# Kernel optimization log

Measured on AMD Instinct MI355X. Metric: run time of the kernel, lower is better.

The kernel has to match this reference:

```python
import jax, jax.numpy as jnp
import numpy as np


def setup_inputs() -> dict:
    key = jax.random.key(0)
    b, d, s = 16, 1024, 4096
    x = jax.random.normal(key, (b, d, s), dtype=jnp.float32)
    return {"x": x, "k": 8}


def reference(x, k):
    # k-max pooling over the last axis, preserving original relative order.
    # torch: topk -> argsort(ind) -> gather. Equivalent: take top-k values,
    # then reorder them by ascending original index.
    vals, idx = jax.lax.top_k(x, k)            # [b, d, k]
    order = jnp.argsort(idx, axis=-1)          # positions that sort original indices ascending
    out = jnp.take_along_axis(vals, order, axis=-1)  # [b, d, k] in original order
    return out
```

## Files before the change

### kernel.cpp

```cpp
#include <hip/hip_runtime.h>
#include <stdint.h>

#define WPB    4
#define CAP    96
#define KK     8
#define SLEN   4096
#define CHUNKS 16

__global__ __launch_bounds__(256, 4)
void kmax_kernel(const float* __restrict__ x, float* __restrict__ out, int nrows) {
    const int wave = threadIdx.x >> 6;
    const int lane = threadIdx.x & 63;
    const int row  = blockIdx.x * WPB + wave;
    const bool active = row < nrows;

    __shared__ int   s_cnt[WPB];
    __shared__ float s_val[WPB][CAP];
    __shared__ int   s_idx[WPB][CAP];

    if (lane == 0) s_cnt[wave] = 0;
    __syncthreads();

    const float NEG_INF = __int_as_float(0xff800000);

    float Tthr = 0.0f;
    float4 f[CHUNKS];

    if (active) {
        const float4* xr = reinterpret_cast<const float4*>(x + (size_t)row * SLEN);
        #pragma unroll
        for (int j = 0; j < CHUNKS; ++j)
            f[j] = xr[j * 64 + lane];

        float m[8];
        #pragma unroll
        for (int e = 0; e < 8; ++e) m[e] = NEG_INF;
        #pragma unroll
        for (int j = 0; j < CHUNKS; ++j) {
            const int b = (j & 1) * 4;
            m[b + 0] = fmaxf(m[b + 0], f[j].x);
            m[b + 1] = fmaxf(m[b + 1], f[j].y);
            m[b + 2] = fmaxf(m[b + 2], f[j].z);
            m[b + 3] = fmaxf(m[b + 3], f[j].w);
        }

        #define MCAS(a, b) { float hi = fmaxf(m[a], m[b]); float lo = fminf(m[a], m[b]); m[a] = hi; m[b] = lo; }
        MCAS(0,1) MCAS(2,3) MCAS(4,5) MCAS(6,7)
        MCAS(0,2) MCAS(1,3) MCAS(4,6) MCAS(5,7)
        MCAS(1,2) MCAS(5,6)
        MCAS(0,4) MCAS(1,5) MCAS(2,6) MCAS(3,7)
        MCAS(2,4) MCAS(3,5)
        MCAS(1,2) MCAS(3,4) MCAS(5,6)
        #undef MCAS

        #pragma unroll
        for (int t = 0; t < KK; ++t) {
            float r = m[0];
            #pragma unroll
            for (int off = 32; off >= 1; off >>= 1)
                r = fmaxf(r, __shfl_xor(r, off, 64));
            const bool win = (m[0] == r);
            m[0] = win ? m[1] : m[0];
            m[1] = win ? m[2] : m[1];
            m[2] = win ? m[3] : m[2];
            m[3] = win ? m[4] : m[3];
            m[4] = win ? m[5] : m[4];
            m[5] = win ? m[6] : m[5];
            m[6] = win ? m[7] : m[6];
            m[7] = win ? NEG_INF : m[7];
            Tthr = r;
        }

        #pragma unroll
        for (int j = 0; j < CHUNKS; ++j) {
            const float4 v = f[j];
            const bool p0 = v.x >= Tthr, p1 = v.y >= Tthr, p2 = v.z >= Tthr, p3 = v.w >= Tthr;
            if (p0 || p1 || p2 || p3) {
                const int base = (j * 64 + lane) * 4;
                if (p0) { int p = atomicAdd(&s_cnt[wave], 1); if (p < CAP) { s_val[wave][p] = v.x; s_idx[wave][p] = base + 0; } }
                if (p1) { int p = atomicAdd(&s_cnt[wave], 1); if (p < CAP) { s_val[wave][p] = v.y; s_idx[wave][p] = base + 1; } }
                if (p2) { int p = atomicAdd(&s_cnt[wave], 1); if (p < CAP) { s_val[wave][p] = v.z; s_idx[wave][p] = base + 2; } }
                if (p3) { int p = atomicAdd(&s_cnt[wave], 1); if (p < CAP) { s_val[wave][p] = v.w; s_idx[wave][p] = base + 3; } }
            }
        }
    }

    __syncthreads();

    if (active) {
        int n = s_cnt[wave];
        if (n > CAP) n = CAP;
        float v  = (lane < n) ? s_val[wave][lane] : NEG_INF;
        int   id = (lane < n) ? s_idx[wave][lane] : 0x7FFFFFFF;

        float rv[KK]; int ri[KK];
        #pragma unroll
        for (int t = 0; t < KK; ++t) {
            float av = v; int ai = id;
            #pragma unroll
            for (int off = 32; off >= 1; off >>= 1) {
                float ov = __shfl_xor(av, off, 64);
                int   oi = __shfl_xor(ai, off, 64);
                const bool take = (ov > av) || (ov == av && oi < ai);
                av = take ? ov : av;
                ai = take ? oi : ai;
            }
            rv[t] = av; ri[t] = ai;
            if (id == ai) v = NEG_INF;
        }

        #define ICAS(a, b) { bool sw = ri[a] > ri[b]; \
            int   tlo = sw ? ri[b] : ri[a]; int   thi = sw ? ri[a] : ri[b]; ri[a] = tlo; ri[b] = thi; \
            float vlo = sw ? rv[b] : rv[a]; float vhi = sw ? rv[a] : rv[b]; rv[a] = vlo; rv[b] = vhi; }
        ICAS(0,1) ICAS(2,3) ICAS(4,5) ICAS(6,7)
        ICAS(0,2) ICAS(1,3) ICAS(4,6) ICAS(5,7)
        ICAS(1,2) ICAS(5,6)
        ICAS(0,4) ICAS(1,5) ICAS(2,6) ICAS(3,7)
        ICAS(2,4) ICAS(3,5)
        ICAS(1,2) ICAS(3,4) ICAS(5,6)
        #undef ICAS

        if (lane == 0) {
            float4* o = reinterpret_cast<float4*>(out + (size_t)row * KK);
            o[0] = make_float4(rv[0], rv[1], rv[2], rv[3]);
            o[1] = make_float4(rv[4], rv[5], rv[6], rv[7]);
        }
    }
}

extern "C" void kernel_launch(void* const* d_in, const int* in_sizes, int n_in,
                              void* d_out, int out_size, void* d_ws, size_t ws_size,
                              hipStream_t stream) {
    const float* x = (const float*)d_in[0];
    float* out = (float*)d_out;
    const int nrows = out_size / KK;
    const int blocks = (nrows + WPB - 1) / WPB;
    kmax_kernel<<<blocks, 256, 0, stream>>>(x, out, nrows);
}
```

Baseline: 358.8 us.

## Use bitonic top-8 merge for threshold and packed 64-bit keys for final selection

Replaces the eight sequential wave-wide max reductions with a butterfly bitonic merge of per-lane sorted top-8 lists. After the merge every lane holds the exact 8th-largest value as its threshold. Candidates are packed into order-preserving 64-bit keys (value bits plus inverted index) in a larger shared buffer. The final top-8 is found by a serial insertion loop that every lane runs redundantly, instead of shuffle-based argmax rounds. This cuts shuffle count and allows more tied candidates, but lowers the occupancy hint, doubles shared memory, and makes the final selection serial in the candidate count.

```diff
diff --git a/kernel.cpp b/kernel.cpp
--- a/kernel.cpp
+++ b/kernel.cpp
@@ -2,32 +2,30 @@
 #include <stdint.h>
 
 #define WPB    4
-#define CAP    96
+#define CAP    256
 #define KK     8
 #define SLEN   4096
 #define CHUNKS 16
 
-__global__ __launch_bounds__(256, 4)
+__global__ __launch_bounds__(256, 3)
 void kmax_kernel(const float* __restrict__ x, float* __restrict__ out, int nrows) {
     const int wave = threadIdx.x >> 6;
     const int lane = threadIdx.x & 63;
     const int row  = blockIdx.x * WPB + wave;
     const bool active = row < nrows;
 
-    __shared__ int   s_cnt[WPB];
-    __shared__ float s_val[WPB][CAP];
-    __shared__ int   s_idx[WPB][CAP];
+    __shared__ int s_cnt[WPB];
+    __shared__ unsigned long long s_key[WPB][CAP];
 
     if (lane == 0) s_cnt[wave] = 0;
     __syncthreads();
 
     const float NEG_INF = __int_as_float(0xff800000);
-
     float Tthr = 0.0f;
-    float4 f[CHUNKS];
 
     if (active) {
         const float4* xr = reinterpret_cast<const float4*>(x + (size_t)row * SLEN);
+        float4 f[CHUNKS];
         #pragma unroll
         for (int j = 0; j < CHUNKS; ++j)
             f[j] = xr[j * 64 + lane];
@@ -54,22 +52,21 @@
         #undef MCAS
 
         #pragma unroll
-        for (int t = 0; t < KK; ++t) {
-            float r = m[0];
+        for (int s = 1; s < 64; s <<= 1) {
+            float b[8], t[8];
             #pragma unroll
-            for (int off = 32; off >= 1; off >>= 1)
-                r = fmaxf(r, __shfl_xor(r, off, 64));
-            const bool win = (m[0] == r);
-            m[0] = win ? m[1] : m[0];
-            m[1] = win ? m[2] : m[1];
-            m[2] = win ? m[3] : m[2];
-            m[3] = win ? m[4] : m[3];
-            m[4] = win ? m[5] : m[4];
-            m[5] = win ? m[6] : m[5];
-            m[6] = win ? m[7] : m[6];
-            m[7] = win ? NEG_INF : m[7];
-            Tthr = r;
+            for (int i = 0; i < 8; ++i) b[i] = __shfl_xor(m[i], s, 64);
+            #pragma unroll
+            for (int i = 0; i < 8; ++i) t[i] = fmaxf(m[i], b[7 - i]);
+            #define BCAS(a, c) { float hi = fmaxf(t[a], t[c]); float lo = fminf(t[a], t[c]); t[a] = hi; t[c] = lo; }
+            BCAS(0,4) BCAS(1,5) BCAS(2,6) BCAS(3,7)
+            BCAS(0,2) BCAS(1,3) BCAS(4,6) BCAS(5,7)
+            BCAS(0,1) BCAS(2,3) BCAS(4,5) BCAS(6,7)
+            #undef BCAS
+            #pragma unroll
+            for (int i = 0; i < 8; ++i) m[i] = t[i];
         }
+        Tthr = m[7];
 
         #pragma unroll
         for (int j = 0; j < CHUNKS; ++j) {
@@ -77,10 +74,18 @@
             const bool p0 = v.x >= Tthr, p1 = v.y >= Tthr, p2 = v.z >= Tthr, p3 = v.w >= Tthr;
             if (p0 || p1 || p2 || p3) {
                 const int base = (j * 64 + lane) * 4;
-                if (p0) { int p = atomicAdd(&s_cnt[wave], 1); if (p < CAP) { s_val[wave][p] = v.x; s_idx[wave][p] = base + 0; } }
-                if (p1) { int p = atomicAdd(&s_cnt[wave], 1); if (p < CAP) { s_val[wave][p] = v.y; s_idx[wave][p] = base + 1; } }
-                if (p2) { int p = atomicAdd(&s_cnt[wave], 1); if (p < CAP) { s_val[wave][p] = v.z; s_idx[wave][p] = base + 2; } }
-                if (p3) { int p = atomicAdd(&s_cnt[wave], 1); if (p < CAP) { s_val[wave][p] = v.w; s_idx[wave][p] = base + 3; } }
+                #define PUSH(val, idx) { \
+                    int p = atomicAdd(&s_cnt[wave], 1); \
+                    if (p < CAP) { \
+                        unsigned u = __float_as_uint(val); \
+                        u ^= ((unsigned)((int)u >> 31)) | 0x80000000u; \
+                        s_key[wave][p] = ((unsigned long long)u << 32) | (unsigned)(4095 - (idx)); \
+                    } }
+                if (p0) PUSH(v.x, base + 0)
+                if (p1) PUSH(v.y, base + 1)
+                if (p2) PUSH(v.z, base + 2)
+                if (p3) PUSH(v.w, base + 3)
+                #undef PUSH
             }
         }
     }
@@ -90,28 +95,24 @@
     if (active) {
         int n = s_cnt[wave];
         if (n > CAP) n = CAP;
-        float v  = (lane < n) ? s_val[wave][lane] : NEG_INF;
-        int   id = (lane < n) ? s_idx[wave][lane] : 0x7FFFFFFF;
 
-        float rv[KK]; int ri[KK];
+        unsigned long long kk[KK];
         #pragma unroll
-        for (int t = 0; t < KK; ++t) {
-            float av = v; int ai = id;
-            #pragma unroll
-            for (int off = 32; off >= 1; off >>= 1) {
-                float ov = __shfl_xor(av, off, 64);
-                int   oi = __shfl_xor(ai, off, 64);
-                const bool take = (ov > av) || (ov == av && oi < ai);
-                av = take ? ov : av;
-                ai = take ? oi : ai;
+        for (int i = 0; i < KK; ++i) kk[i] = 0ull;
+        for (int i = 0; i < n; ++i) {
+            unsigned long long c = s_key[wave][i];
+            if (c > kk[7]) {
+                #pragma unroll
+                for (int t = 7; t > 0; --t)
+                    kk[t] = (c > kk[t - 1]) ? kk[t - 1] : ((c > kk[t]) ? c : kk[t]);
+                kk[0] = (c > kk[0]) ? c : kk[0];
             }
-            rv[t] = av; ri[t] = ai;
-            if (id == ai) v = NEG_INF;
         }
 
-        #define ICAS(a, b) { bool sw = ri[a] > ri[b]; \
-            int   tlo = sw ? ri[b] : ri[a]; int   thi = sw ? ri[a] : ri[b]; ri[a] = tlo; ri[b] = thi; \
-            float vlo = sw ? rv[b] : rv[a]; float vhi = sw ? rv[a] : rv[b]; rv[a] = vlo; rv[b] = vhi; }
+        #define ICAS(a, b) { bool sw = (unsigned)kk[a] < (unsigned)kk[b]; \
+            unsigned long long hi = sw ? kk[b] : kk[a]; \
+            unsigned long long lo = sw ? kk[a] : kk[b]; \
+            kk[a] = hi; kk[b] = lo; }
         ICAS(0,1) ICAS(2,3) ICAS(4,5) ICAS(6,7)
         ICAS(0,2) ICAS(1,3) ICAS(4,6) ICAS(5,7)
         ICAS(1,2) ICAS(5,6)
@@ -121,9 +122,16 @@
         #undef ICAS
 
         if (lane == 0) {
+            float vals[KK];
+            #pragma unroll
+            for (int i = 0; i < KK; ++i) {
+                unsigned g = (unsigned)(kk[i] >> 32);
+                unsigned msk = ((int)g < 0) ? 0x80000000u : 0xFFFFFFFFu;
+                vals[i] = __uint_as_float(g ^ msk);
+            }
             float4* o = reinterpret_cast<float4*>(out + (size_t)row * KK);
-            o[0] = make_float4(rv[0], rv[1], rv[2], rv[3]);
-            o[1] = make_float4(rv[4], rv[5], rv[6], rv[7]);
+            o[0] = make_float4(vals[0], vals[1], vals[2], vals[3]);
+            o[1] = make_float4(vals[4], vals[5], vals[6], vals[7]);
         }
     }
 }
```

Result: no change. 360.1 us (+0.4%).
